# Optimization experiments

Hardware: AMD Instinct MI355X
Metric: run time of the kernel (lower is better)

## Reference

```python
import math
import jax, jax.numpy as jnp
import numpy as np

NUM_HEADS = 32
NUM_KV_HEADS = 8
HEAD_DIM = 128
HIDDEN = 4096
ROPE_THETA = 500000.0
ROPE_FACTOR = 8.0
HIGH_FF = 4.0
LOW_FF = 1.0
ORIG_MAX_POS = 8192


def _llama3_inv_freq():
    # Llama-3 rope frequency scaling
    inv = 1.0 / (ROPE_THETA ** (np.arange(0, HEAD_DIM, 2, dtype=np.float32) / HEAD_DIM))
    wavelen = 2.0 * np.pi / inv
    low_wl = ORIG_MAX_POS / LOW_FF
    high_wl = ORIG_MAX_POS / HIGH_FF
    inv_scaled = np.where(wavelen > low_wl, inv / ROPE_FACTOR, inv)
    smooth = (ORIG_MAX_POS / wavelen - LOW_FF) / (HIGH_FF - LOW_FF)
    smoothed = (1.0 - smooth) / ROPE_FACTOR * inv + smooth * inv
    is_medium = (wavelen <= low_wl) & (wavelen >= high_wl)
    return jnp.asarray(np.where(is_medium, smoothed, inv_scaled), dtype=jnp.float32)


def _rotate_half(x):
    h = x.shape[-1] // 2
    return jnp.concatenate([-x[..., h:], x[..., :h]], axis=-1)


def setup_inputs() -> dict:
    key = jax.random.key(0)
    ks = jax.random.split(key, 5)
    s = 0.02
    return {
        "x": jax.random.normal(ks[0], (1, 2048, HIDDEN), dtype=jnp.float32),
        "Wq": jax.random.normal(ks[1], (NUM_HEADS * HEAD_DIM, HIDDEN), dtype=jnp.float32) * s,
        "Wk": jax.random.normal(ks[2], (NUM_KV_HEADS * HEAD_DIM, HIDDEN), dtype=jnp.float32) * s,
        "Wv": jax.random.normal(ks[3], (NUM_KV_HEADS * HEAD_DIM, HIDDEN), dtype=jnp.float32) * s,
        "Wo": jax.random.normal(ks[4], (HIDDEN, NUM_HEADS * HEAD_DIM), dtype=jnp.float32) * s,
    }


def reference(x, Wq, Wk, Wv, Wo):
    B, T, _ = x.shape
    G = NUM_HEADS // NUM_KV_HEADS  # query heads per kv head

    q = jnp.einsum("bth,oh->bto", x, Wq).reshape(B, T, NUM_HEADS, HEAD_DIM).transpose(0, 2, 1, 3)
    k = jnp.einsum("bth,oh->bto", x, Wk).reshape(B, T, NUM_KV_HEADS, HEAD_DIM).transpose(0, 2, 1, 3)
    v = jnp.einsum("bth,oh->bto", x, Wv).reshape(B, T, NUM_KV_HEADS, HEAD_DIM).transpose(0, 2, 1, 3)

    # RoPE (past_len = 0, prefill)
    inv_freq = _llama3_inv_freq()
    pos = jnp.arange(T, dtype=jnp.float32)
    freqs = pos[:, None] * inv_freq[None, :]             # [T, D/2]
    emb = jnp.concatenate([freqs, freqs], axis=-1)       # [T, D]
    cos, sin = jnp.cos(emb), jnp.sin(emb)
    q = q * cos + _rotate_half(q) * sin
    k = k * cos + _rotate_half(k) * sin

    # GQA attention: group query heads over kv heads instead of repeat_interleave
    qg = q.reshape(B, NUM_KV_HEADS, G, T, HEAD_DIM)
    scale = 1.0 / math.sqrt(HEAD_DIM)
    scores = jnp.einsum("bkgtd,bksd->bkgts", qg, k) * scale  # [B,Hkv,G,T,T]
    causal = jnp.tril(jnp.ones((T, T), dtype=bool))
    scores = jnp.where(causal, scores, -jnp.inf)
    attn = jax.nn.softmax(scores, axis=-1)
    out = jnp.einsum("bkgts,bksd->bkgtd", attn, v)           # [B,Hkv,G,T,D]
    out = out.reshape(B, NUM_HEADS, T, HEAD_DIM).transpose(0, 2, 1, 3).reshape(B, T, NUM_HEADS * HEAD_DIM)
    return jnp.einsum("bto,ho->bth", out, Wo)
```

## Files before the change

kernel.cpp:

```cpp
#include <hip/hip_runtime.h>
#include <math.h>

#define T 2048
#define HID 4096
#define NH 32
#define NKV 8
#define HD 128
#define QSCALE 0.08838834764831845f

typedef __attribute__((ext_vector_type(8))) short short8;
typedef __attribute__((ext_vector_type(4))) float f32x4;
typedef __attribute__((ext_vector_type(16))) float f32x16;

static __device__ __forceinline__ unsigned short f2bf(float f) {
  union { float f; unsigned u; } v; v.f = f;
  unsigned r = v.u;
  r += 0x7fffu + ((r >> 16) & 1u);
  return (unsigned short)(r >> 16);
}

static __device__ __forceinline__ void async_cp16(const unsigned short* g, unsigned short* l) {
  __builtin_amdgcn_global_load_lds(
      (const __attribute__((address_space(1))) void*)g,
      (__attribute__((address_space(3))) void*)l,
      16, 0, 0);
}

__global__ __launch_bounds__(256) void cast4_kernel(const float* __restrict__ s0, const float* __restrict__ s1,
                                                    const float* __restrict__ s2, const float* __restrict__ s3,
                                                    unsigned short* __restrict__ d0, unsigned short* __restrict__ d1,
                                                    unsigned short* __restrict__ d2, unsigned short* __restrict__ d3,
                                                    int n0, int n1, int n2, int n3) {
  int i = blockIdx.x * 256 + threadIdx.x;
  const float* s; unsigned short* d; int j = i;
  if (j < n0) { s = s0; d = d0; }
  else { j -= n0;
    if (j < n1) { s = s1; d = d1; }
    else { j -= n1;
      if (j < n2) { s = s2; d = d2; }
      else { j -= n2;
        if (j >= n3) return;
        s = s3; d = d3; } } }
  float4 f = ((const float4*)s)[j];
  ushort4 o;
  o.x = f2bf(f.x); o.y = f2bf(f.y); o.z = f2bf(f.z); o.w = f2bf(f.w);
  ((ushort4*)d)[j] = o;
}

__global__ __launch_bounds__(256) void cast_bf16_kernel(const float* __restrict__ src,
                                                        unsigned short* __restrict__ dst,
                                                        int n4) {
  int i = blockIdx.x * 256 + threadIdx.x;
  if (i >= n4) return;
  float4 f = ((const float4*)src)[i];
  ushort4 o;
  o.x = f2bf(f.x); o.y = f2bf(f.y); o.z = f2bf(f.z); o.w = f2bf(f.w);
  ((ushort4*)dst)[i] = o;
}

__global__ __launch_bounds__(256) void gemm_bt(const unsigned short* __restrict__ A,
                                               const unsigned short* __restrict__ Bt,
                                               float* __restrict__ C,
                                               int M, int N, int K) {
  __shared__ __align__(16) unsigned short As[128 * 64];
  __shared__ __align__(16) unsigned short Bs[128 * 64];
  int tid = threadIdx.x;
  int wave = tid >> 6, lane = tid & 63;
  int l31 = lane & 31, half = lane >> 5;
  int wr = (wave >> 1) * 64, wc = (wave & 1) * 64;
  long bm0 = (long)blockIdx.y * 128, bn0 = (long)blockIdx.x * 128;
  int lrow8 = lane >> 3;
  int g8 = lane & 7;

  f32x16 acc[2][2] = {};
  for (int k0 = 0; k0 < K; k0 += 64) {
#pragma unroll
    for (int c = 0; c < 4; c++) {
      int chunk = wave * 4 + c;
      int row = chunk * 8 + lrow8;
      int col = (g8 ^ (row & 7)) * 8;
      async_cp16(&A[(bm0 + row) * (long)K + k0 + col], &As[chunk * 512]);
      async_cp16(&Bt[(bn0 + row) * (long)K + k0 + col], &Bs[chunk * 512]);
    }
    __syncthreads();
#pragma unroll
    for (int ks = 0; ks < 4; ks++) {
      short8 af[2], bfr[2];
#pragma unroll
      for (int i = 0; i < 2; i++) {
        int row = wr + i * 32 + l31;
        af[i] = *(const short8*)&As[row * 64 + (((ks * 2 + half) ^ (row & 7)) * 8)];
      }
#pragma unroll
      for (int j = 0; j < 2; j++) {
        int row = wc + j * 32 + l31;
        bfr[j] = *(const short8*)&Bs[row * 64 + (((ks * 2 + half) ^ (row & 7)) * 8)];
      }
#pragma unroll
      for (int i = 0; i < 2; i++)
#pragma unroll
        for (int j = 0; j < 2; j++)
          acc[i][j] = __builtin_amdgcn_mfma_f32_32x32x16_bf16(af[i], bfr[j], acc[i][j], 0, 0, 0);
    }
    __syncthreads();
  }
#pragma unroll
  for (int i = 0; i < 2; i++)
#pragma unroll
    for (int j = 0; j < 2; j++)
#pragma unroll
      for (int r = 0; r < 16; r++) {
        long row = bm0 + wr + i * 32 + (r & 3) + 8 * (r >> 2) + 4 * half;
        long col = bn0 + wc + j * 32 + l31;
        C[row * (long)N + col] = acc[i][j][r];
      }
}

__global__ __launch_bounds__(64) void rope_qk(const float* __restrict__ qkvf,
                                              unsigned short* __restrict__ qb,
                                              unsigned short* __restrict__ kb) {
  int t = blockIdx.x, hh = blockIdx.y, d = threadIdx.x;
  float ex = (float)d * (1.0f / 64.0f);
  float inv = expf(-ex * 13.122363377404328f);
  float wl = 6.283185307179586f / inv;
  float inv_s;
  if (wl > 8192.0f)       inv_s = inv * 0.125f;
  else if (wl < 2048.0f)  inv_s = inv;
  else {
    float smooth = (8192.0f / wl - 1.0f) * (1.0f / 3.0f);
    inv_s = (1.0f - smooth) * 0.125f * inv + smooth * inv;
  }
  float ang = (float)t * inv_s;
  float s, c;
  sincosf(ang, &s, &c);
  if (hh < NH) {
    const float* base = qkvf + (long)t * 6144 + hh * HD;
    float lo = base[d], hi = base[d + 64];
    long o = ((long)hh * T + t) * HD;
    qb[o + d]      = f2bf((lo * c - hi * s) * QSCALE);
    qb[o + d + 64] = f2bf((hi * c + lo * s) * QSCALE);
  } else {
    int h = hh - NH;
    const float* base = qkvf + (long)t * 6144 + 4096 + h * HD;
    float lo = base[d], hi = base[d + 64];
    long o = ((long)h * T + t) * HD;
    kb[o + d]      = f2bf(lo * c - hi * s);
    kb[o + d + 64] = f2bf(hi * c + lo * s);
  }
}

__global__ __launch_bounds__(256) void transpose_v(const float* __restrict__ qkvf,
                                                   unsigned short* __restrict__ vtb) {
  __shared__ float tile[64][33];
  int t0 = blockIdx.x * 64, d0 = blockIdx.y * 32, h = blockIdx.z;
  int tid = threadIdx.x;
  int dd = tid & 31, tt = tid >> 5;
#pragma unroll
  for (int i = 0; i < 8; i++) {
    int t = tt + i * 8;
    tile[t][dd] = qkvf[(long)(t0 + t) * 6144 + 5120 + h * HD + d0 + dd];
  }
  __syncthreads();
  int t2 = tid & 63, d2 = tid >> 6;
#pragma unroll
  for (int i = 0; i < 8; i++) {
    int d = d2 + i * 4;
    vtb[((long)(h * HD + d0 + d)) * T + t0 + t2] = f2bf(tile[t2][d]);
  }
}

__global__ __launch_bounds__(256, 2) void attn_kernel(const unsigned short* __restrict__ qb,
                                                      const unsigned short* __restrict__ kbuf,
                                                      const unsigned short* __restrict__ vtb,
                                                      unsigned short* __restrict__ ob) {
  __shared__ __align__(16) unsigned short Ks[64 * 128];
  __shared__ __align__(16) unsigned short Vs[128 * 64];
  __shared__ __align__(16) unsigned short Ps[4][32 * 76];
  int h = blockIdx.y;
  int kvh = h >> 2;
  int qt = (blockIdx.y >= 16) ? (int)(gridDim.x - 1 - blockIdx.x) : (int)blockIdx.x;
  int q0 = qt * 128;
  int tid = threadIdx.x, wave = tid >> 6, lane = tid & 63;
  int l31 = lane & 31, half = lane >> 5;
  const unsigned short* Kb = kbuf + (long)kvh * T * HD;
  const unsigned short* Vb = vtb + (long)kvh * HD * T;

  int qrow = q0 + wave * 32 + l31;
  short8 aq[8];
#pragma unroll
  for (int ks = 0; ks < 8; ks++)
    aq[ks] = *(const short8*)&qb[((long)h * T + qrow) * HD + ks * 16 + half * 8];

  f32x16 oacc[4] = {};
  float psum[16];
#pragma unroll
  for (int r = 0; r < 16; r++) psum[r] = 0.0f;

  int ntiles = 2 * qt + 2;
  for (int tile = 0; tile < ntiles; tile++) {
    int kb0 = tile * 64;
#pragma unroll
    for (int i = 0; i < 4; i++) {
      int c = wave * 4 + i;
      { int row = c * 4 + (lane >> 4);
        int g = (lane & 15) ^ (row & 15);
        async_cp16(&Kb[(long)(kb0 + row) * HD + g * 8], &Ks[c * 512]); }
      { int row = c * 8 + (lane >> 3);
        int g = (lane & 7) ^ (row & 7);
        async_cp16(&Vb[(long)row * T + kb0 + g * 8], &Vs[c * 512]); }
    }
    __syncthreads();

    f32x16 sacc[2] = {};
#pragma unroll
    for (int ks = 0; ks < 8; ks++)
#pragma unroll
      for (int nt = 0; nt < 2; nt++) {
        int row = nt * 32 + l31;
        short8 bk = *(const short8*)&Ks[row * 128 + (((2 * ks + half) ^ (row & 15)) * 8)];
        sacc[nt] = __builtin_amdgcn_mfma_f32_32x32x16_bf16(aq[ks], bk, sacc[nt], 0, 0, 0);
      }

    if (kb0 + 63 > q0 + wave * 32) {
#pragma unroll
      for (int nt = 0; nt < 2; nt++) {
        int key = kb0 + nt * 32 + l31;
#pragma unroll
        for (int r = 0; r < 16; r++) {
          int qr = q0 + wave * 32 + (r & 3) + 8 * (r >> 2) + 4 * half;
          if (key > qr) sacc[nt][r] = -3.0e38f;
        }
      }
    }

#pragma unroll
    for (int nt = 0; nt < 2; nt++)
#pragma unroll
      for (int r = 0; r < 16; r++) {
        float p = __expf(sacc[nt][r]);
        psum[r] += p;
        int prow = (r & 3) + 8 * (r >> 2) + 4 * half;
        Ps[wave][prow * 76 + nt * 32 + l31] = f2bf(p);
      }

#pragma unroll
    for (int ks = 0; ks < 4; ks++) {
      short8 ap = *(const short8*)&Ps[wave][l31 * 76 + ks * 16 + half * 8];
#pragma unroll
      for (int nt = 0; nt < 4; nt++) {
        int row = nt * 32 + l31;
        short8 bv = *(const short8*)&Vs[row * 64 + (((2 * ks + half) ^ (row & 7)) * 8)];
        oacc[nt] = __builtin_amdgcn_mfma_f32_32x32x16_bf16(ap, bv, oacc[nt], 0, 0, 0);
      }
    }
    __syncthreads();
  }

#pragma unroll
  for (int off = 1; off <= 16; off <<= 1)
#pragma unroll
    for (int r = 0; r < 16; r++)
      psum[r] += __shfl_xor(psum[r], off, 64);

#pragma unroll
  for (int nt = 0; nt < 4; nt++)
#pragma unroll
    for (int r = 0; r < 16; r++) {
      int row = q0 + wave * 32 + (r & 3) + 8 * (r >> 2) + 4 * half;
      ob[(long)row * HID + h * HD + nt * 32 + l31] = f2bf(oacc[nt][r] / psum[r]);
    }
}

extern "C" void kernel_launch(void* const* d_in, const int* in_sizes, int n_in,
                              void* d_out, int out_size, void* d_ws, size_t ws_size,
                              hipStream_t stream) {
  const float* x  = (const float*)d_in[0];
  const float* Wq = (const float*)d_in[1];
  const float* Wk = (const float*)d_in[2];
  const float* Wv = (const float*)d_in[3];
  const float* Wo = (const float*)d_in[4];
  float* out = (float*)d_out;

  char* ws = (char*)d_ws;
  size_t off = 0;
  auto alloc = [&](size_t bytes) {
    char* p = ws + off;
    off += (bytes + 255) & ~(size_t)255;
    return p;
  };
  unsigned short* x_bf    = (unsigned short*)alloc((size_t)T * HID * 2);
  unsigned short* wqkv_bf = (unsigned short*)alloc((size_t)6144 * HID * 2);
  float* qkvf = (float*)alloc((size_t)T * 6144 * 4);
  unsigned short* qb  = (unsigned short*)alloc((size_t)NH * T * HD * 2);
  unsigned short* kbb = (unsigned short*)alloc((size_t)NKV * T * HD * 2);
  unsigned short* vtb = (unsigned short*)alloc((size_t)NKV * HD * T * 2);
  unsigned short* obb = (unsigned short*)alloc((size_t)T * HID * 2);

  int n0 = T * HID / 4, n1 = HID * HID / 4, n2 = 1024 * HID / 4, n3 = 1024 * HID / 4;
  int ntot = n0 + n1 + n2 + n3;
  cast4_kernel<<<dim3((ntot + 255) / 256), dim3(256), 0, stream>>>(
      x, Wq, Wk, Wv,
      x_bf, wqkv_bf, wqkv_bf + (size_t)HID * HID, wqkv_bf + (size_t)5120 * HID,
      n0, n1, n2, n3);

  gemm_bt<<<dim3(6144 / 128, T / 128), dim3(256), 0, stream>>>(x_bf, wqkv_bf, qkvf, T, 6144, HID);

  rope_qk<<<dim3(T, NH + NKV), dim3(64), 0, stream>>>(qkvf, qb, kbb);
  transpose_v<<<dim3(T / 64, HD / 32, NKV), dim3(256), 0, stream>>>(qkvf, vtb);

  cast_bf16_kernel<<<dim3((HID * HID / 4 + 255) / 256), dim3(256), 0, stream>>>(Wo, wqkv_bf, HID * HID / 4);
  attn_kernel<<<dim3(T / 128, NH), dim3(256), 0, stream>>>(qb, kbb, vtb, obb);
  gemm_bt<<<dim3(HID / 128, T / 128), dim3(256), 0, stream>>>(obb, wqkv_bf, out, T, HID, HID);
}
```

Measured before the change: 481.3 us.

## Replace GEMM with 256x256 double-buffered 8-wave pipelined MFMA kernel

Result: slower. 506.8 us (+5.3%).

```diff
diff --git a/kernel.cpp b/kernel.cpp
--- a/kernel.cpp
+++ b/kernel.cpp
@@ -58,62 +58,144 @@
   ((ushort4*)dst)[i] = o;
 }
 
-__global__ __launch_bounds__(256) void gemm_bt(const unsigned short* __restrict__ A,
-                                               const unsigned short* __restrict__ Bt,
-                                               float* __restrict__ C,
-                                               int M, int N, int K) {
-  __shared__ __align__(16) unsigned short As[128 * 64];
-  __shared__ __align__(16) unsigned short Bs[128 * 64];
-  int tid = threadIdx.x;
-  int wave = tid >> 6, lane = tid & 63;
-  int l31 = lane & 31, half = lane >> 5;
-  int wr = (wave >> 1) * 64, wc = (wave & 1) * 64;
-  long bm0 = (long)blockIdx.y * 128, bn0 = (long)blockIdx.x * 128;
-  int lrow8 = lane >> 3;
-  int g8 = lane & 7;
-
-  f32x16 acc[2][2] = {};
-  for (int k0 = 0; k0 < K; k0 += 64) {
-#pragma unroll
-    for (int c = 0; c < 4; c++) {
-      int chunk = wave * 4 + c;
-      int row = chunk * 8 + lrow8;
-      int col = (g8 ^ (row & 7)) * 8;
-      async_cp16(&A[(bm0 + row) * (long)K + k0 + col], &As[chunk * 512]);
-      async_cp16(&Bt[(bn0 + row) * (long)K + k0 + col], &Bs[chunk * 512]);
-    }
-    __syncthreads();
-#pragma unroll
-    for (int ks = 0; ks < 4; ks++) {
-      short8 af[2], bfr[2];
-#pragma unroll
-      for (int i = 0; i < 2; i++) {
-        int row = wr + i * 32 + l31;
-        af[i] = *(const short8*)&As[row * 64 + (((ks * 2 + half) ^ (row & 7)) * 8)];
-      }
-#pragma unroll
-      for (int j = 0; j < 2; j++) {
-        int row = wc + j * 32 + l31;
-        bfr[j] = *(const short8*)&Bs[row * 64 + (((ks * 2 + half) ^ (row & 7)) * 8)];
-      }
-#pragma unroll
-      for (int i = 0; i < 2; i++)
-#pragma unroll
-        for (int j = 0; j < 2; j++)
-          acc[i][j] = __builtin_amdgcn_mfma_f32_32x32x16_bf16(af[i], bfr[j], acc[i][j], 0, 0, 0);
-    }
-    __syncthreads();
-  }
-#pragma unroll
-  for (int i = 0; i < 2; i++)
-#pragma unroll
-    for (int j = 0; j < 2; j++)
-#pragma unroll
-      for (int r = 0; r < 16; r++) {
-        long row = bm0 + wr + i * 32 + (r & 3) + 8 * (r >> 2) + 4 * half;
-        long col = bn0 + wc + j * 32 + l31;
-        C[row * (long)N + col] = acc[i][j][r];
-      }
+
+static __device__ __forceinline__ short8 ldfrag(const unsigned short* tile, int row0, int ks, int lane) {
+  int row = row0 + (lane & 15);
+  int slot = (ks * 4 + (lane >> 4)) ^ (lane & 7);
+  return *(const short8*)&tile[row * 64 + slot * 8];
+}
+
+static __device__ __forceinline__ void stage_half(const unsigned short* __restrict__ G, long grow0, int K, int k0,
+                                                  unsigned short* lds, int h, int wave, int lane) {
+#pragma unroll
+  for (int i = 0; i < 2; i++) {
+    long row = grow0 + h * 128 + i * 64 + wave * 8 + (lane >> 3);
+    int slot = (lane & 7) ^ (lane >> 3);
+    async_cp16(&G[row * (long)K + k0 + slot * 8], &lds[h * 8192 + i * 4096 + wave * 512]);
+  }
+}
+
+template <int MQ, int NQ>
+static __device__ __forceinline__ void mfma_quad(const short8 (&af)[4][2], const short8 (&bf)[2][2],
+                                                 f32x4 (&acc)[8][4]) {
+  __builtin_amdgcn_s_setprio(1);
+#pragma unroll
+  for (int m = 0; m < 4; m++)
+#pragma unroll
+    for (int n = 0; n < 2; n++)
+#pragma unroll
+      for (int ks = 0; ks < 2; ks++)
+        acc[MQ * 4 + m][NQ * 2 + n] = __builtin_amdgcn_mfma_f32_16x16x32_bf16(
+            af[m][ks], bf[n][ks], acc[MQ * 4 + m][NQ * 2 + n], 0, 0, 0);
+  __builtin_amdgcn_s_setprio(0);
+}
+
+#define SCHED0 __builtin_amdgcn_sched_barrier(0)
+#define BAR_PRE  do { SCHED0; __builtin_amdgcn_s_barrier(); \
+                      asm volatile("s_waitcnt lgkmcnt(0)" ::: "memory"); SCHED0; } while (0)
+#define BAR_POST do { SCHED0; __builtin_amdgcn_s_barrier(); SCHED0; } while (0)
+
+__global__ __launch_bounds__(512, 2) void gemm8(const unsigned short* __restrict__ A,
+                                                const unsigned short* __restrict__ Bt,
+                                                float* __restrict__ C,
+                                                int M, int N, int K) {
+  __shared__ __align__(16) unsigned short As[2][16384];
+  __shared__ __align__(16) unsigned short Bs[2][16384];
+  int tid = threadIdx.x, wave = tid >> 6, lane = tid & 63;
+  int wm = wave >> 2, wn = wave & 3;
+  long bm0 = (long)blockIdx.y * 256, bn0 = (long)blockIdx.x * 256;
+  int ar = wm * 128, br = wn * 64;
+
+  f32x4 acc[8][4] = {};
+  short8 a0[4][2], a1[4][2], b0[2][2], b1[2][2];
+
+  stage_half(Bt, bn0, K, 0, Bs[0], 0, wave, lane);
+  stage_half(Bt, bn0, K, 0, Bs[0], 1, wave, lane);
+  stage_half(A,  bm0, K, 0, As[0], 0, wave, lane);
+  stage_half(A,  bm0, K, 0, As[0], 1, wave, lane);
+  stage_half(Bt, bn0, K, 64, Bs[1], 0, wave, lane);
+  stage_half(Bt, bn0, K, 64, Bs[1], 1, wave, lane);
+  asm volatile("s_waitcnt vmcnt(4)" ::: "memory");
+  SCHED0; __builtin_amdgcn_s_barrier(); SCHED0;
+
+  int nkt = K >> 6;
+#pragma unroll 1
+  for (int it = 0; it < (nkt >> 1); ++it) {
+    int k1 = (2 * it + 1) << 6;
+    int t2 = 2 * it + 2; if (t2 > nkt - 1) t2 = nkt - 1;
+    int t3 = 2 * it + 3; if (t3 > nkt - 1) t3 = nkt - 1;
+    int k2 = t2 << 6, k3 = t3 << 6;
+
+#pragma unroll
+    for (int m = 0; m < 4; m++)
+#pragma unroll
+      for (int ks = 0; ks < 2; ks++) a0[m][ks] = ldfrag(As[0], ar + m * 16, ks, lane);
+#pragma unroll
+    for (int n = 0; n < 2; n++)
+#pragma unroll
+      for (int ks = 0; ks < 2; ks++) b0[n][ks] = ldfrag(Bs[0], br + n * 16, ks, lane);
+    stage_half(A, bm0, K, k1, As[1], 0, wave, lane);
+    BAR_PRE; mfma_quad<0, 0>(a0, b0, acc); BAR_POST;
+
+#pragma unroll
+    for (int n = 0; n < 2; n++)
+#pragma unroll
+      for (int ks = 0; ks < 2; ks++) b1[n][ks] = ldfrag(Bs[0], br + (2 + n) * 16, ks, lane);
+    stage_half(A, bm0, K, k1, As[1], 1, wave, lane);
+    BAR_PRE; mfma_quad<0, 1>(a0, b1, acc); BAR_POST;
+
+#pragma unroll
+    for (int m = 0; m < 4; m++)
+#pragma unroll
+      for (int ks = 0; ks < 2; ks++) a1[m][ks] = ldfrag(As[0], ar + (4 + m) * 16, ks, lane);
+    stage_half(Bt, bn0, K, k2, Bs[0], 0, wave, lane);
+    BAR_PRE; mfma_quad<1, 0>(a1, b0, acc); BAR_POST;
+
+    stage_half(Bt, bn0, K, k2, Bs[0], 1, wave, lane);
+    asm volatile("s_waitcnt vmcnt(4)" ::: "memory");
+    BAR_PRE; mfma_quad<1, 1>(a1, b1, acc); BAR_POST;
+
+#pragma unroll
+    for (int m = 0; m < 4; m++)
+#pragma unroll
+      for (int ks = 0; ks < 2; ks++) a0[m][ks] = ldfrag(As[1], ar + m * 16, ks, lane);
+#pragma unroll
+    for (int n = 0; n < 2; n++)
+#pragma unroll
+      for (int ks = 0; ks < 2; ks++) b0[n][ks] = ldfrag(Bs[1], br + n * 16, ks, lane);
+    stage_half(A, bm0, K, k2, As[0], 0, wave, lane);
+    BAR_PRE; mfma_quad<0, 0>(a0, b0, acc); BAR_POST;
+
+#pragma unroll
+    for (int n = 0; n < 2; n++)
+#pragma unroll
+      for (int ks = 0; ks < 2; ks++) b1[n][ks] = ldfrag(Bs[1], br + (2 + n) * 16, ks, lane);
+    stage_half(A, bm0, K, k2, As[0], 1, wave, lane);
+    BAR_PRE; mfma_quad<0, 1>(a0, b1, acc); BAR_POST;
+
+#pragma unroll
+    for (int m = 0; m < 4; m++)
+#pragma unroll
+      for (int ks = 0; ks < 2; ks++) a1[m][ks] = ldfrag(As[1], ar + (4 + m) * 16, ks, lane);
+    stage_half(Bt, bn0, K, k3, Bs[1], 0, wave, lane);
+    BAR_PRE; mfma_quad<1, 0>(a1, b0, acc); BAR_POST;
+
+    stage_half(Bt, bn0, K, k3, Bs[1], 1, wave, lane);
+    asm volatile("s_waitcnt vmcnt(4)" ::: "memory");
+    BAR_PRE; mfma_quad<1, 1>(a1, b1, acc); BAR_POST;
+  }
+  asm volatile("s_waitcnt vmcnt(0)" ::: "memory");
+
+#pragma unroll
+  for (int m = 0; m < 8; m++)
+#pragma unroll
+    for (int n = 0; n < 4; n++) {
+      long row = bm0 + ar + m * 16 + ((lane >> 4) << 2);
+      long col = bn0 + br + n * 16 + (lane & 15);
+#pragma unroll
+      for (int j = 0; j < 4; j++)
+        C[(row + j) * (long)N + col] = acc[m][n][j];
+    }
 }
 
 __global__ __launch_bounds__(64) void rope_qk(const float* __restrict__ qkvf,
@@ -303,12 +385,12 @@
       x_bf, wqkv_bf, wqkv_bf + (size_t)HID * HID, wqkv_bf + (size_t)5120 * HID,
       n0, n1, n2, n3);
 
-  gemm_bt<<<dim3(6144 / 128, T / 128), dim3(256), 0, stream>>>(x_bf, wqkv_bf, qkvf, T, 6144, HID);
+  gemm8<<<dim3(6144 / 256, T / 256), dim3(512), 0, stream>>>(x_bf, wqkv_bf, qkvf, T, 6144, HID);
 
   rope_qk<<<dim3(T, NH + NKV), dim3(64), 0, stream>>>(qkvf, qb, kbb);
   transpose_v<<<dim3(T / 64, HD / 32, NKV), dim3(256), 0, stream>>>(qkvf, vtb);
 
   cast_bf16_kernel<<<dim3((HID * HID / 4 + 255) / 256), dim3(256), 0, stream>>>(Wo, wqkv_bf, HID * HID / 4);
   attn_kernel<<<dim3(T / 128, NH), dim3(256), 0, stream>>>(qb, kbb, vtb, obb);
-  gemm_bt<<<dim3(HID / 128, T / 128), dim3(256), 0, stream>>>(obb, wqkv_bf, out, T, HID, HID);
-}
+  gemm8<<<dim3(HID / 256, T / 256), dim3(512), 0, stream>>>(obb, wqkv_bf, out, T, HID, HID);
+}
```

## Replace GEMM with larger-tile, multi-buffered, software-pipelined MFMA kernel

Applied to the files above, without the earlier changes.

Measured after the change: 461.5 us. -4.1%, faster.

```diff
diff --git a/kernel.cpp b/kernel.cpp
--- a/kernel.cpp
+++ b/kernel.cpp
@@ -58,62 +58,183 @@
   ((ushort4*)dst)[i] = o;
 }
 
-__global__ __launch_bounds__(256) void gemm_bt(const unsigned short* __restrict__ A,
-                                               const unsigned short* __restrict__ Bt,
-                                               float* __restrict__ C,
-                                               int M, int N, int K) {
-  __shared__ __align__(16) unsigned short As[128 * 64];
-  __shared__ __align__(16) unsigned short Bs[128 * 64];
-  int tid = threadIdx.x;
-  int wave = tid >> 6, lane = tid & 63;
-  int l31 = lane & 31, half = lane >> 5;
-  int wr = (wave >> 1) * 64, wc = (wave & 1) * 64;
-  long bm0 = (long)blockIdx.y * 128, bn0 = (long)blockIdx.x * 128;
-  int lrow8 = lane >> 3;
-  int g8 = lane & 7;
-
-  f32x16 acc[2][2] = {};
-  for (int k0 = 0; k0 < K; k0 += 64) {
-#pragma unroll
-    for (int c = 0; c < 4; c++) {
-      int chunk = wave * 4 + c;
-      int row = chunk * 8 + lrow8;
-      int col = (g8 ^ (row & 7)) * 8;
-      async_cp16(&A[(bm0 + row) * (long)K + k0 + col], &As[chunk * 512]);
-      async_cp16(&Bt[(bn0 + row) * (long)K + k0 + col], &Bs[chunk * 512]);
-    }
-    __syncthreads();
-#pragma unroll
-    for (int ks = 0; ks < 4; ks++) {
-      short8 af[2], bfr[2];
-#pragma unroll
-      for (int i = 0; i < 2; i++) {
-        int row = wr + i * 32 + l31;
-        af[i] = *(const short8*)&As[row * 64 + (((ks * 2 + half) ^ (row & 7)) * 8)];
-      }
-#pragma unroll
-      for (int j = 0; j < 2; j++) {
-        int row = wc + j * 32 + l31;
-        bfr[j] = *(const short8*)&Bs[row * 64 + (((ks * 2 + half) ^ (row & 7)) * 8)];
-      }
-#pragma unroll
-      for (int i = 0; i < 2; i++)
-#pragma unroll
-        for (int j = 0; j < 2; j++)
-          acc[i][j] = __builtin_amdgcn_mfma_f32_32x32x16_bf16(af[i], bfr[j], acc[i][j], 0, 0, 0);
-    }
-    __syncthreads();
-  }
-#pragma unroll
-  for (int i = 0; i < 2; i++)
-#pragma unroll
-    for (int j = 0; j < 2; j++)
-#pragma unroll
-      for (int r = 0; r < 16; r++) {
-        long row = bm0 + wr + i * 32 + (r & 3) + 8 * (r >> 2) + 4 * half;
-        long col = bn0 + wc + j * 32 + l31;
-        C[row * (long)N + col] = acc[i][j][r];
-      }
+
+static __device__ __forceinline__ short8 ldfrag(const unsigned short* tile, int row0, int ks, int lane) {
+  int row = row0 + (lane & 15);
+  int slot = (ks * 4 + (lane >> 4)) ^ (lane & 7);
+  return *(const short8*)&tile[row * 64 + slot * 8];
+}
+
+static __device__ __forceinline__ void ldb2(short8 (&b)[2][2], const unsigned short* bs, int br0, int lane) {
+#pragma unroll
+  for (int j = 0; j < 2; j++)
+#pragma unroll
+    for (int ks = 0; ks < 2; ks++)
+      b[j][ks] = ldfrag(bs, br0 + j * 16, ks, lane);
+}
+
+template <int H>
+static __device__ __forceinline__ void preA(short8 (&a)[4][2], const unsigned short* as, int ar, int lane) {
+#pragma unroll
+  for (int m = 2 * H; m < 2 * H + 2; m++)
+#pragma unroll
+    for (int ks = 0; ks < 2; ks++)
+      a[m][ks] = ldfrag(as, ar + m * 16, ks, lane);
+}
+
+template <int P, int NF>
+static __device__ __forceinline__ void mfma16(const short8 (&a)[4][2], const short8 (&b)[2][2],
+                                              f32x4 (&acc)[4][2 * NF]) {
+  __builtin_amdgcn_s_setprio(1);
+#pragma unroll
+  for (int ks = 0; ks < 2; ks++)
+#pragma unroll
+    for (int m = 0; m < 4; m++)
+#pragma unroll
+      for (int j = 0; j < 2; j++)
+        acc[m][P * 2 + j] = __builtin_amdgcn_mfma_f32_16x16x32_bf16(
+            a[m][ks], b[j][ks], acc[m][P * 2 + j], 0, 0, 0);
+  __builtin_amdgcn_s_setprio(0);
+}
+
+#define SCHED0 __builtin_amdgcn_sched_barrier(0)
+#define BAR_PRE  do { SCHED0; __builtin_amdgcn_s_barrier(); \
+                      asm volatile("s_waitcnt lgkmcnt(0)" ::: "memory"); SCHED0; } while (0)
+#define BAR_POST do { SCHED0; __builtin_amdgcn_s_barrier(); SCHED0; } while (0)
+#define VMCNT(n) asm volatile("s_waitcnt vmcnt(" #n ")" ::: "memory")
+
+template <int NF>
+static __device__ __forceinline__ void tile_body(
+    short8 (&aC)[4][2], short8 (&aN)[4][2],
+    const unsigned short* bsRd, unsigned short* bsSt,
+    const unsigned short* asN, unsigned short* asS,
+    const unsigned short* const (&baseA)[4], const unsigned short* const (&baseB)[NF],
+    int kA, int kB, int ar, int br, int wave, int lane,
+    f32x4 (&acc)[4][2 * NF]) {
+  short8 b[2][2];
+  if constexpr (NF == 3) {
+    ldb2(b, bsRd, br + 0, lane);
+    async_cp16(baseB[0] + kB, bsSt + 0 * 4096 + wave * 512);
+    async_cp16(baseB[1] + kB, bsSt + 1 * 4096 + wave * 512);
+    async_cp16(baseB[2] + kB, bsSt + 2 * 4096 + wave * 512);
+    BAR_PRE; mfma16<0, NF>(aC, b, acc); BAR_POST;
+    ldb2(b, bsRd, br + 32, lane);
+    preA<0>(aN, asN, ar, lane);
+    async_cp16(baseA[0] + kA, asS + 0 * 4096 + wave * 512);
+    async_cp16(baseA[1] + kA, asS + 1 * 4096 + wave * 512);
+    BAR_PRE; mfma16<1, NF>(aC, b, acc); BAR_POST;
+    ldb2(b, bsRd, br + 64, lane);
+    preA<1>(aN, asN, ar, lane);
+    async_cp16(baseA[2] + kA, asS + 2 * 4096 + wave * 512);
+    async_cp16(baseA[3] + kA, asS + 3 * 4096 + wave * 512);
+    VMCNT(4);
+    BAR_PRE; mfma16<2, NF>(aC, b, acc); BAR_POST;
+  } else {
+    ldb2(b, bsRd, br + 0, lane);
+    preA<0>(aN, asN, ar, lane);
+    async_cp16(baseB[0] + kB, bsSt + 0 * 4096 + wave * 512);
+    async_cp16(baseB[1] + kB, bsSt + 1 * 4096 + wave * 512);
+    BAR_PRE; mfma16<0, NF>(aC, b, acc); BAR_POST;
+    ldb2(b, bsRd, br + 32, lane);
+    preA<1>(aN, asN, ar, lane);
+    async_cp16(baseA[0] + kA, asS + 0 * 4096 + wave * 512);
+    async_cp16(baseA[1] + kA, asS + 1 * 4096 + wave * 512);
+    async_cp16(baseA[2] + kA, asS + 2 * 4096 + wave * 512);
+    async_cp16(baseA[3] + kA, asS + 3 * 4096 + wave * 512);
+    VMCNT(6);
+    BAR_PRE; mfma16<1, NF>(aC, b, acc); BAR_POST;
+  }
+}
+
+template <int NF>
+__global__ __launch_bounds__(512, 2) void gemm9(const unsigned short* __restrict__ A,
+                                                const unsigned short* __restrict__ Bt,
+                                                float* __restrict__ C,
+                                                int M, int N, int K) {
+  __shared__ __align__(16) unsigned short AsBuf[3][16384];
+  __shared__ __align__(16) unsigned short BsBuf[NF == 3 ? 2 : 3][NF * 4096];
+  int tid = threadIdx.x, wave = tid >> 6, lane = tid & 63;
+  int wm = wave >> 1, wn = wave & 1;
+  long bm0 = (long)blockIdx.y * 256, bn0 = (long)blockIdx.x * (NF * 64);
+  int ar = wm * 64, br = wn * (NF * 32);
+
+  long stRow = wave * 8 + (lane >> 3);
+  int slot = ((lane & 7) ^ (lane >> 3)) * 8;
+  const unsigned short* baseA[4];
+#pragma unroll
+  for (int c = 0; c < 4; c++) baseA[c] = A + (bm0 + c * 64 + stRow) * (long)K + slot;
+  const unsigned short* baseB[NF];
+#pragma unroll
+  for (int c = 0; c < NF; c++) baseB[c] = Bt + (bn0 + c * 64 + stRow) * (long)K + slot;
+
+  int nkt = K >> 6;
+  f32x4 acc[4][2 * NF] = {};
+  short8 aX[4][2], aY[4][2];
+  unsigned short *as0 = AsBuf[0], *as1 = AsBuf[1], *as2 = AsBuf[2];
+
+  if constexpr (NF == 3) {
+#pragma unroll
+    for (int c = 0; c < 3; c++) async_cp16(baseB[c], &BsBuf[0][c * 4096 + wave * 512]);
+#pragma unroll
+    for (int c = 0; c < 4; c++) async_cp16(baseA[c], as0 + c * 4096 + wave * 512);
+#pragma unroll
+    for (int c = 0; c < 4; c++) async_cp16(baseA[c] + 64, as1 + c * 4096 + wave * 512);
+#pragma unroll
+    for (int c = 0; c < 4; c++) async_cp16(baseA[c] + 128, as2 + c * 4096 + wave * 512);
+    VMCNT(4);
+    SCHED0; __builtin_amdgcn_s_barrier(); SCHED0;
+    preA<0>(aX, as0, ar, lane); preA<1>(aX, as0, ar, lane);
+#pragma unroll 1
+    for (int it = 0; it < (nkt >> 1); ++it) {
+      int t = 2 * it;
+      int kA0 = ((t + 3) < nkt ? (t + 3) : (nkt - 1)) << 6;
+      int kB0 = ((t + 1) < nkt ? (t + 1) : (nkt - 1)) << 6;
+      tile_body<3>(aX, aY, BsBuf[0], BsBuf[1], as1, as0, baseA, baseB, kA0, kB0, ar, br, wave, lane, acc);
+      int kA1 = ((t + 4) < nkt ? (t + 4) : (nkt - 1)) << 6;
+      int kB1 = ((t + 2) < nkt ? (t + 2) : (nkt - 1)) << 6;
+      tile_body<3>(aY, aX, BsBuf[1], BsBuf[0], as2, as1, baseA, baseB, kA1, kB1, ar, br, wave, lane, acc);
+      unsigned short* tA = as0; as0 = as2; as2 = as1; as1 = tA;
+    }
+  } else {
+    unsigned short *bs0 = BsBuf[0], *bs1 = BsBuf[1], *bs2 = BsBuf[2];
+#pragma unroll
+    for (int c = 0; c < 2; c++) async_cp16(baseB[c], bs0 + c * 4096 + wave * 512);
+#pragma unroll
+    for (int c = 0; c < 4; c++) async_cp16(baseA[c], as0 + c * 4096 + wave * 512);
+#pragma unroll
+    for (int c = 0; c < 2; c++) async_cp16(baseB[c] + 64, bs1 + c * 4096 + wave * 512);
+#pragma unroll
+    for (int c = 0; c < 4; c++) async_cp16(baseA[c] + 64, as1 + c * 4096 + wave * 512);
+#pragma unroll
+    for (int c = 0; c < 4; c++) async_cp16(baseA[c] + 128, as2 + c * 4096 + wave * 512);
+    VMCNT(4);
+    SCHED0; __builtin_amdgcn_s_barrier(); SCHED0;
+    preA<0>(aX, as0, ar, lane); preA<1>(aX, as0, ar, lane);
+#pragma unroll 1
+    for (int it = 0; it < (nkt >> 1); ++it) {
+      int t = 2 * it;
+      int kA0 = ((t + 3) < nkt ? (t + 3) : (nkt - 1)) << 6;
+      int kB0 = ((t + 2) < nkt ? (t + 2) : (nkt - 1)) << 6;
+      tile_body<2>(aX, aY, bs0, bs2, as1, as0, baseA, baseB, kA0, kB0, ar, br, wave, lane, acc);
+      int kA1 = ((t + 4) < nkt ? (t + 4) : (nkt - 1)) << 6;
+      int kB1 = ((t + 3) < nkt ? (t + 3) : (nkt - 1)) << 6;
+      tile_body<2>(aY, aX, bs1, bs0, as2, as1, baseA, baseB, kA1, kB1, ar, br, wave, lane, acc);
+      unsigned short* tA = as0; as0 = as2; as2 = as1; as1 = tA;
+      unsigned short* tB = bs0; bs0 = bs2; bs2 = bs1; bs1 = tB;
+    }
+  }
+  VMCNT(0);
+
+#pragma unroll
+  for (int m = 0; m < 4; m++)
+#pragma unroll
+    for (int n = 0; n < 2 * NF; n++) {
+      long row = bm0 + ar + m * 16 + ((lane >> 4) << 2);
+      long col = bn0 + br + n * 16 + (lane & 15);
+#pragma unroll
+      for (int j = 0; j < 4; j++)
+        C[(row + j) * (long)N + col] = acc[m][n][j];
+    }
 }
 
 __global__ __launch_bounds__(64) void rope_qk(const float* __restrict__ qkvf,
@@ -303,12 +424,12 @@
       x_bf, wqkv_bf, wqkv_bf + (size_t)HID * HID, wqkv_bf + (size_t)5120 * HID,
       n0, n1, n2, n3);
 
-  gemm_bt<<<dim3(6144 / 128, T / 128), dim3(256), 0, stream>>>(x_bf, wqkv_bf, qkvf, T, 6144, HID);
+  gemm9<3><<<dim3(6144 / 192, T / 256), dim3(512), 0, stream>>>(x_bf, wqkv_bf, qkvf, T, 6144, HID);
 
   rope_qk<<<dim3(T, NH + NKV), dim3(64), 0, stream>>>(qkvf, qb, kbb);
   transpose_v<<<dim3(T / 64, HD / 32, NKV), dim3(256), 0, stream>>>(qkvf, vtb);
 
   cast_bf16_kernel<<<dim3((HID * HID / 4 + 255) / 256), dim3(256), 0, stream>>>(Wo, wqkv_bf, HID * HID / 4);
   attn_kernel<<<dim3(T / 128, NH), dim3(256), 0, stream>>>(qb, kbb, vtb, obb);
-  gemm_bt<<<dim3(HID / 128, T / 128), dim3(256), 0, stream>>>(obb, wqkv_bf, out, T, HID, HID);
-}
+  gemm9<2><<<dim3(HID / 128, T / 256), dim3(512), 0, stream>>>(obb, wqkv_bf, out, T, HID, HID);
+}
```
